# Kernel optimization log

Hardware: AMD Instinct MI355X
Metric: run time of the kernel (lower is better)

Reference implementation:

```python
import jax, jax.numpy as jnp
import numpy as np

H = 1024
B, S = 8, 2048

def setup_inputs() -> dict:
    key = jax.random.key(0)
    ks = jax.random.split(key, 7)
    inputs = jax.random.normal(ks[0], (B, S, H), dtype=jnp.float32)
    mask = jnp.ones((B, S), dtype=jnp.int32)
    sc = 1.0 / np.sqrt(H)
    Wq = jax.random.normal(ks[1], (H, H), dtype=jnp.float32) * sc
    bq = jnp.zeros((H,), dtype=jnp.float32)
    Wk = jax.random.normal(ks[2], (H, H), dtype=jnp.float32) * sc
    bk = jnp.zeros((H,), dtype=jnp.float32)
    Wv = jax.random.normal(ks[3], (H, H), dtype=jnp.float32) * sc
    bv = jnp.zeros((H,), dtype=jnp.float32)
    return {"inputs": inputs, "mask": mask, "Wq": Wq, "bq": bq, "Wk": Wk, "bk": bk, "Wv": Wv, "bv": bv}

def reference(inputs, mask, Wq, bq, Wk, bk, Wv, bv):
    scale = jnp.asarray(H ** 0.5, inputs.dtype)
    q = jnp.einsum('bsh,hd->bsd', inputs, Wq) + bq
    k = jnp.einsum('bsh,hd->bsd', inputs, Wk) + bk
    v = jnp.einsum('bsh,hd->bsd', inputs, Wv) + bv
    scores = jnp.einsum('bqd,bkd->bqk', q, k) / scale  # [B,S,S]
    scores = jnp.where(mask[:, None, :] == 0, -jnp.inf, scores)
    attn = jax.nn.softmax(scores, axis=-1)
    return jnp.einsum('bqk,bkd->bqd', attn, v)
```

## Files before the change

kernel.cpp:

```cpp
#include <hip/hip_runtime.h>
#include <stdint.h>

#define DEVI __device__ __forceinline__

typedef __bf16 bf16x8 __attribute__((ext_vector_type(8)));
typedef float  floatx4 __attribute__((ext_vector_type(4)));


DEVI unsigned short f2bf(float f) {
  union { float f; uint32_t u; } x; x.f = f;
  return (unsigned short)((x.u + 0x7fffu + ((x.u >> 16) & 1u)) >> 16);
}
DEVI float bf2f(unsigned short s) {
  union { uint32_t u; float f; } x; x.u = ((uint32_t)s) << 16;
  return x.f;
}

__global__ __launch_bounds__(256) void k_prep(
    const float* __restrict__ X, unsigned short* __restrict__ Xb,
    const float* __restrict__ Wq, const float* __restrict__ Wk,
    const float* __restrict__ Wv, unsigned short* __restrict__ Wt,
    float* __restrict__ lvec) {
  __shared__ float tile[64][65];
  int bx = blockIdx.x, t = threadIdx.x;
  if (bx < 16384) {
    int i = bx * 256 + t;
    float4 v = ((const float4*)X)[i];
    ushort4 o;
    o.x = f2bf(v.x); o.y = f2bf(v.y); o.z = f2bf(v.z); o.w = f2bf(v.w);
    ((ushort4*)Xb)[i] = o;
  } else if (bx < 17152) {
    int idx = bx - 16384;
    int sel = idx >> 8, b2 = idx & 255;
    const float* W = sel == 0 ? Wq : (sel == 1 ? Wk : Wv);
    unsigned short* Wo = Wt + ((size_t)sel << 20);
    int h0 = (b2 & 15) * 64, d0 = (b2 >> 4) * 64;
#pragma unroll
    for (int i = 0; i < 16; ++i) {
      int idx2 = i * 256 + t; int r = idx2 >> 6, c = idx2 & 63;
      tile[r][c] = W[(size_t)(h0 + r) * 1024 + d0 + c];
    }
    __syncthreads();
#pragma unroll
    for (int i = 0; i < 16; ++i) {
      int idx2 = i * 256 + t; int r = idx2 >> 6, c = idx2 & 63;
      Wo[(size_t)(d0 + r) * 1024 + h0 + c] = f2bf(tile[c][r]);
    }
  } else {
    float4 z4 = {0.f, 0.f, 0.f, 0.f};
#pragma unroll
    for (int i = 0; i < 16; ++i) ((float4*)lvec)[i * 256 + t] = z4;
  }
}

DEVI void gl_lds16(const unsigned short* gp, const unsigned short* lp) {
  __builtin_amdgcn_global_load_lds(
      (const __attribute__((address_space(1))) void*)gp,
      (__attribute__((address_space(3))) void*)lp, 16, 0, 0);
}

#define STAGE_A(q, BUF)                                                       \
  do {                                                                        \
    gl_lds16(gA[q][0], AsF + (BUF) + dA[q][0]);                               \
    gl_lds16(gA[q][1], AsF + (BUF) + dA[q][1]);                               \
    gA[q][0] += 64; gA[q][1] += 64;                                           \
  } while (0)
#define STAGE_B(q, BUF)                                                       \
  do {                                                                        \
    gl_lds16(gB[q][0], BsF + (BUF) + dB[q][0]);                               \
    gl_lds16(gB[q][1], BsF + (BUF) + dB[q][1]);                               \
    gB[q][0] += 64; gB[q][1] += 64;                                           \
  } while (0)

#define READ_A(MH)                                                            \
  _Pragma("unroll") for (int ms = 0; ms < 4; ++ms) {                          \
    af[0][ms] = *(const bf16x8*)(pA0 + (MH) * 8192 + ms * 2048);              \
    af[1][ms] = *(const bf16x8*)(pA1 + (MH) * 8192 + ms * 2048);              \
  }
#define READ_B(DST, NH)                                                       \
  _Pragma("unroll") for (int ns = 0; ns < 2; ++ns) {                          \
    DST[0][ns] = *(const bf16x8*)(pB0 + (NH) * 4096 + ns * 2048);             \
    DST[1][ns] = *(const bf16x8*)(pB1 + (NH) * 4096 + ns * 2048);             \
  }

#define MFMA_Q(MH, NH, BSET)                                                  \
  _Pragma("unroll") for (int kk = 0; kk < 2; ++kk)                            \
  _Pragma("unroll") for (int ms = 0; ms < 4; ++ms)                            \
  _Pragma("unroll") for (int ns = 0; ns < 2; ++ns)                            \
    acc[(MH) * 4 + ms][(NH) * 2 + ns] =                                       \
        __builtin_amdgcn_mfma_f32_16x16x32_bf16(                              \
            af[kk][ms], BSET[kk][ns], acc[(MH) * 4 + ms][(NH) * 2 + ns],      \
            0, 0, 0);

#define PRIO1 __builtin_amdgcn_s_setprio(1)
#define PRIO0 __builtin_amdgcn_s_setprio(0)
#define WAITV4 asm volatile("s_waitcnt vmcnt(4)" ::: "memory")
#define WAITV0 asm volatile("s_waitcnt vmcnt(0)" ::: "memory")
#define SBAR __builtin_amdgcn_s_barrier()

template <int EPI>
__global__ __launch_bounds__(512, 2) void k_gemm(
    const unsigned short* __restrict__ A, const unsigned short* __restrict__ Bt,
    void* __restrict__ Cv,
    const float* __restrict__ bias_q, const float* __restrict__ bias_k,
    const float* __restrict__ bias_v,
    const float* __restrict__ lvec, float* __restrict__ lsum,
    const int* __restrict__ mask,
    long aZ, long bZ, int ldA, int ldB, int kIters)
{
  __shared__ __attribute__((aligned(16))) unsigned short AsF[2 * 256 * 64];
  __shared__ __attribute__((aligned(16))) unsigned short BsF[2 * 256 * 64];
  const int tid = threadIdx.x, w = tid >> 6, l = tid & 63;
  const int quad = l >> 4, l15 = l & 15;
  const int wr = w & 1, wc = w >> 1;
  const int wm = wr * 128, wn = wc * 64;
  const int m0 = blockIdx.x * 256;
  const int z = blockIdx.z;

  int n0, sel = 0;
  if constexpr (EPI == 4) { sel = blockIdx.y >> 2; n0 = (blockIdx.y & 3) * 256; }
  else n0 = blockIdx.y * 256;

  const unsigned short* Az = A + (size_t)z * aZ;
  const unsigned short* Bz = (EPI == 4) ? (Bt + ((size_t)sel << 20))
                                        : (Bt + (size_t)z * bZ);

  const int lr = l >> 3, uu = (l & 7) ^ lr;
  const unsigned short* gA[2][2]; const unsigned short* gB[2][2];
  int dA[2][2], dB[2][2];
#pragma unroll
  for (int q = 0; q < 2; ++q)
#pragma unroll
    for (int j = 0; j < 2; ++j) {
      int slot = w * 2 + j;
      int rA = (slot >> 3) * 128 + q * 64 + (slot & 7) * 8;
      int rB = (slot >> 2) * 64 + q * 32 + (slot & 3) * 8;
      gA[q][j] = Az + (size_t)(m0 + rA + lr) * ldA + uu * 8;
      gB[q][j] = Bz + (size_t)(n0 + rB + lr) * ldB + uu * 8;
      dA[q][j] = rA * 64; dB[q][j] = rB * 64;
    }

  const int cc0 = quad ^ (l15 & 7), cc1 = cc0 ^ 4;
  const int aoffA0 = (wm + l15) * 128 + cc0 * 16;
  const int aoffA1 = (wm + l15) * 128 + cc1 * 16;
  const int aoffB0 = (wn + l15) * 128 + cc0 * 16;
  const int aoffB1 = (wn + l15) * 128 + cc1 * 16;

  floatx4 acc[8][4];
#pragma unroll
  for (int i = 0; i < 8; ++i)
#pragma unroll
    for (int j = 0; j < 4; ++j) { floatx4 zz = {0.f, 0.f, 0.f, 0.f}; acc[i][j] = zz; }

  STAGE_A(0, 0); STAGE_B(0, 0);
  STAGE_A(1, 0); STAGE_B(1, 0);
  if (kIters > 1) {
    STAGE_A(0, 16384); STAGE_B(0, 16384);
    WAITV4;
  } else {
    WAITV0;
  }
  SBAR;

#pragma unroll 2
  for (int kt = 0; kt < kIters; ++kt) {
    const int ob = (kt & 1) ? 16384 : 0;
    const int on = ob ^ 16384;
    const char* pA0 = (const char*)(AsF + ob) + aoffA0;
    const char* pA1 = (const char*)(AsF + ob) + aoffA1;
    const char* pB0 = (const char*)(BsF + ob) + aoffB0;
    const char* pB1 = (const char*)(BsF + ob) + aoffB1;
    bf16x8 af[2][4], bfr0[2][2], bfr1[2][2];

    READ_A(0); READ_B(bfr0, 0); READ_B(bfr1, 1);
    if (kt + 1 < kIters) { STAGE_A(1, on); STAGE_B(1, on); }
    SBAR;
    PRIO1;
    MFMA_Q(0, 0, bfr0);
    MFMA_Q(0, 1, bfr1);
    PRIO0;
    SBAR;
    READ_A(1);
    if (kt + 2 < kIters) { STAGE_A(0, ob); STAGE_B(0, ob); }
    SBAR;
    PRIO1;
    MFMA_Q(1, 1, bfr1);
    MFMA_Q(1, 0, bfr0);
    PRIO0;
    if (kt + 2 < kIters) { WAITV4; } else { WAITV0; }
    SBAR;
  }

  if constexpr (EPI == 4) {
    unsigned short* C = (unsigned short*)Cv + ((size_t)sel << 24);
    const float* bs = sel == 0 ? bias_q : (sel == 1 ? bias_k : bias_v);
    if (sel < 2) {
      float sc = sel == 0 ? 0.045084439f : 1.0f;
#pragma unroll
      for (int ns = 0; ns < 4; ++ns) {
        int n_g = n0 + wn + ns * 16 + l15;
        float bv = bs[n_g];
#pragma unroll
        for (int ms = 0; ms < 8; ++ms) {
          int mb = m0 + wm + ms * 16 + quad * 4;
#pragma unroll
          for (int r = 0; r < 4; ++r)
            C[(size_t)(mb + r) * 1024 + n_g] = f2bf((acc[ms][ns][r] + bv) * sc);
        }
      }
    } else {
#pragma unroll
      for (int ns = 0; ns < 4; ++ns) {
        int n_g = n0 + wn + ns * 16 + l15;
        float bv = bs[n_g];
#pragma unroll
        for (int ms = 0; ms < 8; ++ms) {
          int m_g = m0 + wm + ms * 16 + quad * 4;
          int bb = m_g >> 11, key = m_g & 2047;
          ushort4 pk;
          pk.x = f2bf(acc[ms][ns][0] + bv);
          pk.y = f2bf(acc[ms][ns][1] + bv);
          pk.z = f2bf(acc[ms][ns][2] + bv);
          pk.w = f2bf(acc[ms][ns][3] + bv);
          *(ushort4*)&C[((size_t)bb << 21) + ((size_t)n_g << 11) + key] = pk;
        }
      }
    }
  } else if constexpr (EPI == 2) {
    unsigned short* C = (unsigned short*)Cv + (size_t)z * 4194304;
    const int* mz = mask + z * 2048;
    float rowsum[8][4];
#pragma unroll
    for (int ms = 0; ms < 8; ++ms)
#pragma unroll
      for (int r = 0; r < 4; ++r) rowsum[ms][r] = 0.f;
#pragma unroll
    for (int ns = 0; ns < 4; ++ns) {
      int n_g = n0 + wn + ns * 16 + l15;
      int mv = mz[n_g];
#pragma unroll
      for (int ms = 0; ms < 8; ++ms) {
#pragma unroll
        for (int r = 0; r < 4; ++r) {
          int m_g = m0 + wm + ms * 16 + quad * 4 + r;
          float e;
          asm("v_exp_f32 %0, %1" : "=v"(e) : "v"(acc[ms][ns][r]));
          e = mv ? e : 0.f;
          unsigned short pb = f2bf(e);
          C[(size_t)m_g * 2048 + n_g] = pb;
          rowsum[ms][r] += bf2f(pb);
        }
      }
    }
#pragma unroll
    for (int ms = 0; ms < 8; ++ms) {
#pragma unroll
      for (int r = 0; r < 4; ++r) {
        float s = rowsum[ms][r];
#pragma unroll
        for (int off = 1; off < 16; off <<= 1) s += __shfl_xor(s, off);
        if (l15 == 0) {
          int m_g = m0 + wm + ms * 16 + quad * 4 + r;
          atomicAdd(&lsum[z * 2048 + m_g], s);
        }
      }
    }
  } else {
    float* C = (float*)Cv + (size_t)z * 2048 * 1024;
    const float* lz = lvec + z * 2048;
#pragma unroll
    for (int ms = 0; ms < 8; ++ms) {
#pragma unroll
      for (int r = 0; r < 4; ++r) {
        int m_g = m0 + wm + ms * 16 + quad * 4 + r;
        float lw = lz[m_g];
        float inv = lw > 0.f ? 1.f / lw : 0.f;
#pragma unroll
        for (int ns = 0; ns < 4; ++ns) {
          int n_g = n0 + wn + ns * 16 + l15;
          C[(size_t)m_g * 1024 + n_g] = acc[ms][ns][r] * inv;
        }
      }
    }
  }
}

extern "C" void kernel_launch(void* const* d_in, const int* in_sizes, int n_in,
                              void* d_out, int out_size, void* d_ws, size_t ws_size,
                              hipStream_t stream) {
  const float* X    = (const float*)d_in[0];
  const int*   mask = (const int*)d_in[1];
  const float* Wq   = (const float*)d_in[2];
  const float* bq   = (const float*)d_in[3];
  const float* Wk   = (const float*)d_in[4];
  const float* bk   = (const float*)d_in[5];
  const float* Wv   = (const float*)d_in[6];
  const float* bv   = (const float*)d_in[7];
  float* out = (float*)d_out;

  constexpr size_t SZ = (size_t)16384 * 1024;
  unsigned short* Q    = (unsigned short*)d_ws;
  float*          lvec = (float*)(Q + 3 * SZ);
  unsigned short* P    = (unsigned short*)(lvec + 16384);
  unsigned short* Xb   = P;
  unsigned short* Wt   = Xb + SZ;
  unsigned short* Vt   = Q + 2 * SZ;

  k_prep<<<dim3(17153), 256, 0, stream>>>(X, Xb, Wq, Wk, Wv, Wt, lvec);

  k_gemm<4><<<dim3(64, 12, 1), 512, 0, stream>>>(
      Xb, Wt, (void*)Q, bq, bk, bv, nullptr, nullptr, nullptr,
      0, 0, 1024, 1024, 16);

  k_gemm<2><<<dim3(8, 8, 8), 512, 0, stream>>>(
      Q, Q + SZ, (void*)P, nullptr, nullptr, nullptr, nullptr, lvec, mask,
      2048 * 1024, 2048 * 1024, 1024, 1024, 16);

  k_gemm<3><<<dim3(8, 4, 8), 512, 0, stream>>>(
      P, Vt, (void*)out, nullptr, nullptr, nullptr, lvec, nullptr, nullptr,
      2048 * 2048, 1024 * 2048, 2048, 2048, 32);
}
```

Before: 401.8 us.

## Restructure GEMM main loop into four MFMA phases with prefetched B fragments

Splits each k-iteration of the bf16 GEMM into four quadrant phases. The global-to-LDS staging of the A and B halves is interleaved across them, and the first B fragment for the next iteration is loaded from LDS early and carried in registers. The aim is finer overlap of LDS reads, global loads and MFMA work, and fewer register live ranges per phase. It adds more barriers and explicit lgkmcnt waits, and the vmcnt accounting for the staged loads is more intricate, so ordering errors or added stalls are possible.

```diff
diff --git a/kernel.cpp b/kernel.cpp
--- a/kernel.cpp
+++ b/kernel.cpp
@@ -77,11 +77,6 @@
     af[0][ms] = *(const bf16x8*)(pA0 + (MH) * 8192 + ms * 2048);              \
     af[1][ms] = *(const bf16x8*)(pA1 + (MH) * 8192 + ms * 2048);              \
   }
-#define READ_B(DST, NH)                                                       \
-  _Pragma("unroll") for (int ns = 0; ns < 2; ++ns) {                          \
-    DST[0][ns] = *(const bf16x8*)(pB0 + (NH) * 4096 + ns * 2048);             \
-    DST[1][ns] = *(const bf16x8*)(pB1 + (NH) * 4096 + ns * 2048);             \
-  }
 
 #define MFMA_Q(MH, NH, BSET)                                                  \
   _Pragma("unroll") for (int kk = 0; kk < 2; ++kk)                            \
@@ -95,8 +90,14 @@
 #define PRIO1 __builtin_amdgcn_s_setprio(1)
 #define PRIO0 __builtin_amdgcn_s_setprio(0)
 #define WAITV4 asm volatile("s_waitcnt vmcnt(4)" ::: "memory")
+#define WAITV2 asm volatile("s_waitcnt vmcnt(2)" ::: "memory")
 #define WAITV0 asm volatile("s_waitcnt vmcnt(0)" ::: "memory")
 #define SBAR __builtin_amdgcn_s_barrier()
+#define LGK0                                                                  \
+  do {                                                                        \
+    asm volatile("s_waitcnt lgkmcnt(0)" ::: "memory");                        \
+    __builtin_amdgcn_sched_barrier(0);                                        \
+  } while (0)
 
 template <int EPI>
 __global__ __launch_bounds__(512, 2) void k_gemm(
@@ -162,6 +163,16 @@
   }
   SBAR;
 
+  bf16x8 b0[2][2];
+  {
+    const char* qB0 = (const char*)AsF;
+    (void)qB0;
+    const char* rB0 = (const char*)BsF + aoffB0;
+    const char* rB1 = (const char*)BsF + aoffB1;
+    b0[0][0] = *(const bf16x8*)(rB0); b0[0][1] = *(const bf16x8*)(rB0 + 2048);
+    b0[1][0] = *(const bf16x8*)(rB1); b0[1][1] = *(const bf16x8*)(rB1 + 2048);
+  }
+
 #pragma unroll 2
   for (int kt = 0; kt < kIters; ++kt) {
     const int ob = (kt & 1) ? 16384 : 0;
@@ -170,25 +181,42 @@
     const char* pA1 = (const char*)(AsF + ob) + aoffA1;
     const char* pB0 = (const char*)(BsF + ob) + aoffB0;
     const char* pB1 = (const char*)(BsF + ob) + aoffB1;
-    bf16x8 af[2][4], bfr0[2][2], bfr1[2][2];
-
-    READ_A(0); READ_B(bfr0, 0); READ_B(bfr1, 1);
-    if (kt + 1 < kIters) { STAGE_A(1, on); STAGE_B(1, on); }
-    SBAR;
-    PRIO1;
-    MFMA_Q(0, 0, bfr0);
-    MFMA_Q(0, 1, bfr1);
-    PRIO0;
+    bf16x8 af[2][4], bfr1[2][2], b0n[2][2];
+
+    READ_A(0);
+    if (kt + 1 < kIters) STAGE_A(1, on);
+    SBAR; LGK0;
+    PRIO1; MFMA_Q(0, 0, b0); PRIO0;
+    SBAR;
+    bfr1[0][0] = *(const bf16x8*)(pB0 + 4096);
+    bfr1[0][1] = *(const bf16x8*)(pB0 + 4096 + 2048);
+    bfr1[1][0] = *(const bf16x8*)(pB1 + 4096);
+    bfr1[1][1] = *(const bf16x8*)(pB1 + 4096 + 2048);
+    if (kt + 1 < kIters) STAGE_B(1, on);
+    SBAR; LGK0;
+    PRIO1; MFMA_Q(0, 1, bfr1); PRIO0;
     SBAR;
     READ_A(1);
-    if (kt + 2 < kIters) { STAGE_A(0, ob); STAGE_B(0, ob); }
-    SBAR;
-    PRIO1;
-    MFMA_Q(1, 1, bfr1);
-    MFMA_Q(1, 0, bfr0);
-    PRIO0;
+    if (kt + 2 < kIters) STAGE_A(0, ob);
+    SBAR; LGK0;
+    PRIO1; MFMA_Q(1, 1, bfr1); PRIO0;
+    if (kt + 2 < kIters) { WAITV4; } else if (kt + 1 < kIters) { WAITV2; }
+    SBAR;
+    if (kt + 1 < kIters) {
+      const char* qB0 = (const char*)(BsF + on) + aoffB0;
+      const char* qB1 = (const char*)(BsF + on) + aoffB1;
+      b0n[0][0] = *(const bf16x8*)(qB0); b0n[0][1] = *(const bf16x8*)(qB0 + 2048);
+      b0n[1][0] = *(const bf16x8*)(qB1); b0n[1][1] = *(const bf16x8*)(qB1 + 2048);
+    }
+    if (kt + 2 < kIters) STAGE_B(0, ob);
+    SBAR;
+    PRIO1; MFMA_Q(1, 0, b0); PRIO0;
     if (kt + 2 < kIters) { WAITV4; } else { WAITV0; }
     SBAR;
+    if (kt + 1 < kIters) {
+      b0[0][0] = b0n[0][0]; b0[0][1] = b0n[0][1];
+      b0[1][0] = b0n[1][0]; b0[1][1] = b0n[1][1];
+    }
   }
 
   if constexpr (EPI == 4) {
```

New measurement: 406.9 us. About the same (+1.3%).

## Restructure GEMM main loop into four-phase software pipeline with register prefetch

Applied to the files above, without the earlier changes.

Reworks the bf16 MFMA GEMM main loop into four barrier-separated phases. Each phase interleaves async global-to-LDS staging, LDS reads of the next operand fragments into a second register set, and MFMA on the current fragments, with explicit lgkmcnt/vmcnt waits and sched_barrier fences. Global addresses are recomputed from byte offsets instead of being kept as per-thread incremented pointers, which is meant to free registers. The goal is to hide LDS read latency behind MFMA work, at the cost of more barriers and extra fragment registers that could raise register pressure.

```diff
diff --git a/kernel.cpp b/kernel.cpp
--- a/kernel.cpp
+++ b/kernel.cpp
@@ -59,44 +59,55 @@
       (__attribute__((address_space(3))) void*)lp, 16, 0, 0);
 }
 
-#define STAGE_A(q, BUF)                                                       \
-  do {                                                                        \
-    gl_lds16(gA[q][0], AsF + (BUF) + dA[q][0]);                               \
-    gl_lds16(gA[q][1], AsF + (BUF) + dA[q][1]);                               \
-    gA[q][0] += 64; gA[q][1] += 64;                                           \
-  } while (0)
-#define STAGE_B(q, BUF)                                                       \
-  do {                                                                        \
-    gl_lds16(gB[q][0], BsF + (BUF) + dB[q][0]);                               \
-    gl_lds16(gB[q][1], BsF + (BUF) + dB[q][1]);                               \
-    gB[q][0] += 64; gB[q][1] += 64;                                           \
-  } while (0)
-
-#define READ_A(MH)                                                            \
+#define STAGE_A(q, BUF, KT)                                                   \
+  _Pragma("unroll") for (int j = 0; j < 2; ++j) {                             \
+    const int slot = w * 2 + j;                                               \
+    const int rA = (slot >> 3) * 128 + (q) * 64 + (slot & 7) * 8;             \
+    gl_lds16((const unsigned short*)(AzByte +                                 \
+             (size_t)(unsigned)((m0 + rA) * ldA) * 2 + (KT) * 128 + laneA),   \
+             AsF + (BUF) + rA * 64);                                          \
+  }
+#define STAGE_B(q, BUF, KT)                                                   \
+  _Pragma("unroll") for (int j = 0; j < 2; ++j) {                             \
+    const int slot = w * 2 + j;                                               \
+    const int rB = (slot >> 2) * 64 + (q) * 32 + (slot & 3) * 8;              \
+    gl_lds16((const unsigned short*)(BzByte +                                 \
+             (size_t)(unsigned)((n0 + rB) * ldB) * 2 + (KT) * 128 + laneB),   \
+             BsF + (BUF) + rB * 64);                                          \
+  }
+
+#define READ_AF(dst, bp0, bp1, MH)                                            \
   _Pragma("unroll") for (int ms = 0; ms < 4; ++ms) {                          \
-    af[0][ms] = *(const bf16x8*)(pA0 + (MH) * 8192 + ms * 2048);              \
-    af[1][ms] = *(const bf16x8*)(pA1 + (MH) * 8192 + ms * 2048);              \
-  }
-#define READ_B(DST, NH)                                                       \
+    dst[0][ms] = *(const bf16x8*)((bp0) + (MH) * 8192 + ms * 2048);           \
+    dst[1][ms] = *(const bf16x8*)((bp1) + (MH) * 8192 + ms * 2048);           \
+  }
+#define READ_BF(dst, bp0, bp1, NH)                                            \
   _Pragma("unroll") for (int ns = 0; ns < 2; ++ns) {                          \
-    DST[0][ns] = *(const bf16x8*)(pB0 + (NH) * 4096 + ns * 2048);             \
-    DST[1][ns] = *(const bf16x8*)(pB1 + (NH) * 4096 + ns * 2048);             \
-  }
-
-#define MFMA_Q(MH, NH, BSET)                                                  \
+    dst[0][ns] = *(const bf16x8*)((bp0) + (NH) * 4096 + ns * 2048);           \
+    dst[1][ns] = *(const bf16x8*)((bp1) + (NH) * 4096 + ns * 2048);           \
+  }
+
+#define MFMA_Q(ASET, BSET, MH, NH)                                            \
   _Pragma("unroll") for (int kk = 0; kk < 2; ++kk)                            \
   _Pragma("unroll") for (int ms = 0; ms < 4; ++ms)                            \
   _Pragma("unroll") for (int ns = 0; ns < 2; ++ns)                            \
     acc[(MH) * 4 + ms][(NH) * 2 + ns] =                                       \
         __builtin_amdgcn_mfma_f32_16x16x32_bf16(                              \
-            af[kk][ms], BSET[kk][ns], acc[(MH) * 4 + ms][(NH) * 2 + ns],      \
+            ASET[kk][ms], BSET[kk][ns], acc[(MH) * 4 + ms][(NH) * 2 + ns],    \
             0, 0, 0);
 
 #define PRIO1 __builtin_amdgcn_s_setprio(1)
 #define PRIO0 __builtin_amdgcn_s_setprio(0)
+#define WAITV6 asm volatile("s_waitcnt vmcnt(6)" ::: "memory")
 #define WAITV4 asm volatile("s_waitcnt vmcnt(4)" ::: "memory")
 #define WAITV0 asm volatile("s_waitcnt vmcnt(0)" ::: "memory")
 #define SBAR __builtin_amdgcn_s_barrier()
+#define FENCE __builtin_amdgcn_sched_barrier(0)
+#define LGK0                                                                  \
+  do {                                                                        \
+    asm volatile("s_waitcnt lgkmcnt(0)" ::: "memory");                        \
+    __builtin_amdgcn_sched_barrier(0);                                        \
+  } while (0)
 
 template <int EPI>
 __global__ __launch_bounds__(512, 2) void k_gemm(
@@ -124,21 +135,12 @@
   const unsigned short* Az = A + (size_t)z * aZ;
   const unsigned short* Bz = (EPI == 4) ? (Bt + ((size_t)sel << 20))
                                         : (Bt + (size_t)z * bZ);
+  const char* AzByte = (const char*)Az;
+  const char* BzByte = (const char*)Bz;
 
   const int lr = l >> 3, uu = (l & 7) ^ lr;
-  const unsigned short* gA[2][2]; const unsigned short* gB[2][2];
-  int dA[2][2], dB[2][2];
-#pragma unroll
-  for (int q = 0; q < 2; ++q)
-#pragma unroll
-    for (int j = 0; j < 2; ++j) {
-      int slot = w * 2 + j;
-      int rA = (slot >> 3) * 128 + q * 64 + (slot & 7) * 8;
-      int rB = (slot >> 2) * 64 + q * 32 + (slot & 3) * 8;
-      gA[q][j] = Az + (size_t)(m0 + rA + lr) * ldA + uu * 8;
-      gB[q][j] = Bz + (size_t)(n0 + rB + lr) * ldB + uu * 8;
-      dA[q][j] = rA * 64; dB[q][j] = rB * 64;
-    }
+  const int laneA = (lr * ldA + uu * 8) * 2;
+  const int laneB = (lr * ldB + uu * 8) * 2;
 
   const int cc0 = quad ^ (l15 & 7), cc1 = cc0 ^ 4;
   const int aoffA0 = (wm + l15) * 128 + cc0 * 16;
@@ -152,43 +154,71 @@
 #pragma unroll
     for (int j = 0; j < 4; ++j) { floatx4 zz = {0.f, 0.f, 0.f, 0.f}; acc[i][j] = zz; }
 
-  STAGE_A(0, 0); STAGE_B(0, 0);
-  STAGE_A(1, 0); STAGE_B(1, 0);
+  STAGE_A(0, 0, 0); STAGE_B(0, 0, 0);
+  STAGE_A(1, 0, 0); STAGE_B(1, 0, 0);
   if (kIters > 1) {
-    STAGE_A(0, 16384); STAGE_B(0, 16384);
+    STAGE_A(0, 16384, 1); STAGE_B(0, 16384, 1);
     WAITV4;
   } else {
     WAITV0;
   }
   SBAR;
+
+  bf16x8 af0[2][4], af1[2][4], b0[2][2], b1[2][2], b0n[2][2];
+  {
+    const char* cA0 = (const char*)AsF + aoffA0;
+    const char* cA1 = (const char*)AsF + aoffA1;
+    const char* cB0 = (const char*)BsF + aoffB0;
+    const char* cB1 = (const char*)BsF + aoffB1;
+    READ_AF(af0, cA0, cA1, 0);
+    READ_BF(b0,  cB0, cB1, 0);
+  }
 
 #pragma unroll 2
   for (int kt = 0; kt < kIters; ++kt) {
     const int ob = (kt & 1) ? 16384 : 0;
     const int on = ob ^ 16384;
-    const char* pA0 = (const char*)(AsF + ob) + aoffA0;
-    const char* pA1 = (const char*)(AsF + ob) + aoffA1;
-    const char* pB0 = (const char*)(BsF + ob) + aoffB0;
-    const char* pB1 = (const char*)(BsF + ob) + aoffB1;
-    bf16x8 af[2][4], bfr0[2][2], bfr1[2][2];
-
-    READ_A(0); READ_B(bfr0, 0); READ_B(bfr1, 1);
-    if (kt + 1 < kIters) { STAGE_A(1, on); STAGE_B(1, on); }
-    SBAR;
-    PRIO1;
-    MFMA_Q(0, 0, bfr0);
-    MFMA_Q(0, 1, bfr1);
-    PRIO0;
-    SBAR;
-    READ_A(1);
-    if (kt + 2 < kIters) { STAGE_A(0, ob); STAGE_B(0, ob); }
-    SBAR;
-    PRIO1;
-    MFMA_Q(1, 1, bfr1);
-    MFMA_Q(1, 0, bfr0);
-    PRIO0;
-    if (kt + 2 < kIters) { WAITV4; } else { WAITV0; }
-    SBAR;
+    const char* cA0 = (const char*)(AsF + ob) + aoffA0;
+    const char* cA1 = (const char*)(AsF + ob) + aoffA1;
+    const char* cB0 = (const char*)(BsF + ob) + aoffB0;
+    const char* cB1 = (const char*)(BsF + ob) + aoffB1;
+    const char* nA0 = (const char*)(AsF + on) + aoffA0;
+    const char* nA1 = (const char*)(AsF + on) + aoffA1;
+    const char* nB0 = (const char*)(BsF + on) + aoffB0;
+    const char* nB1 = (const char*)(BsF + on) + aoffB1;
+    const bool s1 = kt + 1 < kIters, s2 = kt + 2 < kIters;
+
+    SBAR; LGK0;
+    if (s1) STAGE_A(1, on, kt + 1);
+    READ_BF(b1, cB0, cB1, 1);
+    FENCE;
+    PRIO1; MFMA_Q(af0, b0, 0, 0); PRIO0;
+
+    SBAR; LGK0;
+    if (s1) STAGE_B(1, on, kt + 1);
+    READ_AF(af1, cA0, cA1, 1);
+    FENCE;
+    PRIO1; MFMA_Q(af0, b1, 0, 1); PRIO0;
+    if (s1) WAITV6;
+
+    SBAR; LGK0;
+    if (s2) STAGE_A(0, ob, kt + 2);
+    if (s1) READ_AF(af0, nA0, nA1, 0);
+    FENCE;
+    PRIO1; MFMA_Q(af1, b1, 1, 1); PRIO0;
+    if (s2) { WAITV6; } else if (s1) { WAITV0; }
+
+    SBAR; LGK0;
+    if (s2) STAGE_B(0, ob, kt + 2);
+    if (s1) READ_BF(b0n, nB0, nB1, 0);
+    FENCE;
+    PRIO1; MFMA_Q(af1, b0, 1, 0); PRIO0;
+    if (s2) WAITV4;
+
+    if (s1) {
+      b0[0][0] = b0n[0][0]; b0[0][1] = b0n[0][1];
+      b0[1][0] = b0n[1][0]; b0[1][1] = b0n[1][1];
+    }
   }
 
   if constexpr (EPI == 4) {
```

Result: slower. 725.1 us (+80.5%).

## Stage GEMM epilogues through LDS for vector stores and remap blocks per XCD

Applied to the files above, without the earlier changes.

Each wave now writes its bf16 epilogue tile (QK projection, transposed V, and exp-scores) into a private LDS slice, then writes it to global memory as 16-byte vectors. This replaces scattered 2-byte and 8-byte stores. Separately, the block indices for the score and PV GEMMs are remapped so that blocks landing on the same XCD share A/B tiles, which should improve L2 reuse. The cost is extra LDS traffic in the epilogue and a dependence on the grid shape assumed by the remap.

```diff
diff --git a/kernel.cpp b/kernel.cpp
--- a/kernel.cpp
+++ b/kernel.cpp
@@ -108,18 +108,34 @@
     const int* __restrict__ mask,
     long aZ, long bZ, int ldA, int ldB, int kIters)
 {
-  __shared__ __attribute__((aligned(16))) unsigned short AsF[2 * 256 * 64];
-  __shared__ __attribute__((aligned(16))) unsigned short BsF[2 * 256 * 64];
+  __shared__ __attribute__((aligned(16))) unsigned short LDSu[4 * 256 * 64];
+  unsigned short* const AsF = LDSu;
+  unsigned short* const BsF = LDSu + 2 * 256 * 64;
   const int tid = threadIdx.x, w = tid >> 6, l = tid & 63;
   const int quad = l >> 4, l15 = l & 15;
   const int wr = w & 1, wc = w >> 1;
   const int wm = wr * 128, wn = wc * 64;
-  const int m0 = blockIdx.x * 256;
-  const int z = blockIdx.z;
+
+  int bx = blockIdx.x, by = blockIdx.y, bz = blockIdx.z;
+  if constexpr (EPI == 2) {
+    int lin = bx + (by << 3) + (bz << 6);
+    int xcd = lin & 7, slot = lin >> 3;
+    bx = ((xcd & 1) << 2) + (slot & 3);
+    by = ((xcd >> 1) << 1) + ((slot >> 2) & 1);
+    bz = slot >> 3;
+  } else if constexpr (EPI == 3) {
+    int lin = bx + (by << 3) + (bz << 5);
+    int xcd = lin & 7, slot = lin >> 3;
+    bx = ((xcd & 3) << 1) + (slot & 1);
+    by = ((xcd >> 2) << 1) + ((slot >> 1) & 1);
+    bz = slot >> 2;
+  }
+  const int m0 = bx * 256;
+  const int z = bz;
 
   int n0, sel = 0;
-  if constexpr (EPI == 4) { sel = blockIdx.y >> 2; n0 = (blockIdx.y & 3) * 256; }
-  else n0 = blockIdx.y * 256;
+  if constexpr (EPI == 4) { sel = by >> 2; n0 = (by & 3) * 256; }
+  else n0 = by * 256;
 
   const unsigned short* Az = A + (size_t)z * aZ;
   const unsigned short* Bz = (EPI == 4) ? (Bt + ((size_t)sel << 20))
@@ -194,6 +210,7 @@
   if constexpr (EPI == 4) {
     unsigned short* C = (unsigned short*)Cv + ((size_t)sel << 24);
     const float* bs = sel == 0 ? bias_q : (sel == 1 ? bias_k : bias_v);
+    unsigned short* sl = LDSu + w * 8192;
     if (sel < 2) {
       float sc = sel == 0 ? 0.045084439f : 1.0f;
 #pragma unroll
@@ -202,11 +219,16 @@
         float bv = bs[n_g];
 #pragma unroll
         for (int ms = 0; ms < 8; ++ms) {
-          int mb = m0 + wm + ms * 16 + quad * 4;
+          int lrow = ms * 16 + quad * 4;
 #pragma unroll
           for (int r = 0; r < 4; ++r)
-            C[(size_t)(mb + r) * 1024 + n_g] = f2bf((acc[ms][ns][r] + bv) * sc);
-        }
+            sl[(lrow + r) * 64 + ns * 16 + l15] = f2bf((acc[ms][ns][r] + bv) * sc);
+        }
+      }
+#pragma unroll
+      for (int i = 0; i < 16; ++i) {
+        bf16x8 v = *(const bf16x8*)&sl[i * 512 + l * 8];
+        *(bf16x8*)&C[(size_t)(m0 + wm + i * 8 + lr) * 1024 + n0 + wn + (l & 7) * 8] = v;
       }
     } else {
 #pragma unroll
@@ -215,20 +237,26 @@
         float bv = bs[n_g];
 #pragma unroll
         for (int ms = 0; ms < 8; ++ms) {
-          int m_g = m0 + wm + ms * 16 + quad * 4;
-          int bb = m_g >> 11, key = m_g & 2047;
           ushort4 pk;
           pk.x = f2bf(acc[ms][ns][0] + bv);
           pk.y = f2bf(acc[ms][ns][1] + bv);
           pk.z = f2bf(acc[ms][ns][2] + bv);
           pk.w = f2bf(acc[ms][ns][3] + bv);
-          *(ushort4*)&C[((size_t)bb << 21) + ((size_t)n_g << 11) + key] = pk;
-        }
+          *(ushort4*)&sl[(ns * 16 + l15) * 128 + ms * 16 + quad * 4] = pk;
+        }
+      }
+      const size_t vbase = ((size_t)(m0 >> 11) << 21) + (size_t)((m0 & 2047) + wm);
+#pragma unroll
+      for (int i = 0; i < 16; ++i) {
+        bf16x8 v = *(const bf16x8*)&sl[i * 512 + l * 8];
+        int drow = n0 + wn + i * 4 + quad;
+        *(bf16x8*)&C[vbase + ((size_t)drow << 11) + (l & 15) * 8] = v;
       }
     }
   } else if constexpr (EPI == 2) {
     unsigned short* C = (unsigned short*)Cv + (size_t)z * 4194304;
     const int* mz = mask + z * 2048;
+    unsigned short* sl = LDSu + w * 8192;
     float rowsum[8][4];
 #pragma unroll
     for (int ms = 0; ms < 8; ++ms)
@@ -240,14 +268,14 @@
       int mv = mz[n_g];
 #pragma unroll
       for (int ms = 0; ms < 8; ++ms) {
+        int lrow = ms * 16 + quad * 4;
 #pragma unroll
         for (int r = 0; r < 4; ++r) {
-          int m_g = m0 + wm + ms * 16 + quad * 4 + r;
           float e;
           asm("v_exp_f32 %0, %1" : "=v"(e) : "v"(acc[ms][ns][r]));
           e = mv ? e : 0.f;
           unsigned short pb = f2bf(e);
-          C[(size_t)m_g * 2048 + n_g] = pb;
+          sl[(lrow + r) * 64 + ns * 16 + l15] = pb;
           rowsum[ms][r] += bf2f(pb);
         }
       }
@@ -264,6 +292,11 @@
           atomicAdd(&lsum[z * 2048 + m_g], s);
         }
       }
+    }
+#pragma unroll
+    for (int i = 0; i < 16; ++i) {
+      bf16x8 v = *(const bf16x8*)&sl[i * 512 + l * 8];
+      *(bf16x8*)&C[(size_t)(m0 + wm + i * 8 + lr) * 2048 + n0 + wn + (l & 7) * 8] = v;
     }
   } else {
     float* C = (float*)Cv + (size_t)z * 2048 * 1024;
```

New measurement: 378.5 us. -5.8%, faster.
